# Performance work log

Measured on AMD Instinct MI355X. Metric: run time of the kernel, lower is better.

Reference implementation:

```python
import jax, jax.numpy as jnp
import numpy as np

N = 65536        # collocation points
IN_DIM = 4       # x_dim=3 + is_unsteady=1
DEPTH = 256      # hidden width ('depth' arg)
HID = 5          # width-1 hidden tanh layers
OUT = 3


def setup_inputs() -> dict:
    key = jax.random.key(0)
    ks = jax.random.split(key, 4)
    def init(k, shape, fan_in):
        return jax.random.normal(k, shape, dtype=jnp.float32) / np.sqrt(fan_in).astype(np.float32)
    return {
        "x":  jax.random.normal(ks[0], (N, IN_DIM), dtype=jnp.float32),
        "W0": init(ks[1], (IN_DIM, DEPTH), IN_DIM),
        "b0": jnp.zeros((DEPTH,), jnp.float32),
        "Wh": init(ks[2], (HID, DEPTH, DEPTH), DEPTH),
        "bh": jnp.zeros((HID, DEPTH), jnp.float32),
        "Wl": init(ks[3], (DEPTH, OUT), DEPTH),
        "bl": jnp.zeros((OUT,), jnp.float32),
    }


def _mlp(x, W0, b0, Wh, bh, Wl, bl):
    # Faithful to nn.Sequential: first Linear has NO activation after it,
    # then (width-1) x [Linear, Tanh], then output Linear.
    h = x @ W0 + b0
    for i in range(HID):
        h = jnp.tanh(h @ Wh[i] + bh[i])
    return h @ Wl + bl  # vector potential a: [N, 3]


def reference(x, W0, b0, Wh, bh, Wl, bl):
    # curl(a) via 3 batched reverse-mode pulls (same math as torch autograd.grad
    # with grad_outputs = e_i repeated over the batch).
    a, vjp_fn = jax.vjp(lambda xx: _mlp(xx, W0, b0, Wh, bh, Wl, bl), x)
    e = jnp.eye(OUT, dtype=x.dtype)
    cots = jnp.broadcast_to(e[:, None, :], (OUT, x.shape[0], OUT))  # [3, N, 3]
    J = jax.vmap(lambda c: vjp_fn(c)[0])(cots)                      # [3, N, IN_DIM]
    da0dx, da1dx, da2dx = J[0], J[1], J[2]
    u = jnp.stack([
        da2dx[:, 1] - da1dx[:, 2],
        da0dx[:, 2] - da2dx[:, 0],
        da1dx[:, 0] - da0dx[:, 1],
    ], axis=1)  # [N, 3]
    return u
```

## Files before the change

### kernel.cpp

```cpp
#include <hip/hip_runtime.h>

typedef _Float16 f16;
typedef _Float16 f16x8 __attribute__((ext_vector_type(8)));
typedef float    f32x4 __attribute__((ext_vector_type(4)));

#define OFF_WHP   0u
#define OFF_WLP   655360u
#define OFF_W0P   663552u
#define OFF_B0P   729088u
#define OFF_GP    745472u
#define OFF_BHP   794624u

__device__ __forceinline__ int phi(int kk, int g, int e){
  return (kk*2 + (e>>2))*16 + g*4 + (e&3);
}

__device__ __forceinline__ float tanh_fast(float z){
  float e = __builtin_amdgcn_exp2f(z * 2.885390081777927f);
  return 1.f - 2.f*__builtin_amdgcn_rcpf(e + 1.f);
}

__global__ void prepack(const float* __restrict__ W0, const float* __restrict__ b0,
                        const float* __restrict__ Wh, const float* __restrict__ bh,
                        const float* __restrict__ Wl, unsigned char* __restrict__ ws){
  int tid = blockIdx.x*256 + threadIdx.x;
  f16*   whp = (f16*)(ws + OFF_WHP);
  f16*   wlp = (f16*)(ws + OFF_WLP);
  float* w0p = (float*)(ws + OFF_W0P);
  float* b0p = (float*)(ws + OFF_B0P);
  float* gp  = (float*)(ws + OFF_GP);
  float* bhp = (float*)(ws + OFF_BHP);
  if (tid < 327680){
    int e=tid&7, lane=(tid>>3)&63, kk=(tid>>9)&7, nt=(tid>>12)&15, l=tid>>16;
    int k = phi(kk, lane>>4, e);
    int n = nt*16 + (lane&15);
    whp[tid] = (f16)Wh[(l*256 + k)*256 + n];
  } else if (tid < 331776){
    int t = tid - 327680;
    int e=t&7, lane=(t>>3)&63, kk=t>>9;
    int k = phi(kk, lane>>4, e);
    int n = lane&15;
    wlp[t] = (n<3) ? (f16)Wl[k*3+n] : (f16)0.f;
  } else if (tid < 335872){
    int t = tid - 331776;
    int e=t&7, lane=(t>>3)&63, kk=t>>9;
    int k = phi(kk, lane>>4, e);
    #pragma unroll
    for(int i=0;i<4;i++) w0p[t*4+i] = W0[i*256+k];
    b0p[t] = b0[k];
  } else if (tid < 348160){
    int t = tid - 335872;
    int e=t&7, lane=(t>>3)&63, kk=(t>>9)&7, j=t>>12;
    int k = phi(kk, lane>>4, e);
    float acc = 0.f;
    for(int k0=0;k0<256;k0++) acc = fmaf(W0[j*256+k0], Wh[k0*256+k], acc);
    gp[t] = acc;
  } else if (tid < 368640){
    int t = tid - 348160;
    int r=t&3, lane=(t>>2)&63, nt=(t>>8)&15, l=t>>12;
    bhp[t] = bh[l*256 + nt*16 + (lane>>4)*4 + r];
  }
}

__device__ __forceinline__ int moff(int lane, int kk){
  return lane*128 + ((kk ^ (lane & 7)) << 4);
}

__global__ __launch_bounds__(512, 4) void velcurl(
    const float* __restrict__ x, const unsigned char* __restrict__ ws,
    float* __restrict__ out){
  __shared__ __align__(16) char xbuf[4][8192];
  __shared__ __align__(16) char mbuf[2][8192];
  __shared__ float outt[3][3][16];

  const int lane  = threadIdx.x & 63;
  const int W     = threadIdx.x >> 6;
  const int c     = W & 3;
  const int h     = W >> 2;
  const int s     = lane & 15;
  const int sbase = blockIdx.x << 4;

  const f16x8* __restrict__ whp = (const f16x8*)(ws + OFF_WHP);
  const f16x8* __restrict__ wlp = (const f16x8*)(ws + OFF_WLP);
  const f32x4* __restrict__ w0p = (const f32x4*)(ws + OFF_W0P);
  const float* __restrict__ b0p = (const float*)(ws + OFF_B0P);
  const float* __restrict__ gp  = (const float*)(ws + OFF_GP);
  const f32x4* __restrict__ bhp = (const f32x4*)(ws + OFF_BHP);

  f16x8 st[8];

  if (c==0){
    const f32x4 xv = ((const f32x4*)x)[sbase + s];
    #pragma unroll
    for(int kk=0;kk<8;kk++){
      f16x8 v;
      #pragma unroll
      for(int e=0;e<8;e++){
        f32x4 wv = w0p[(kk*64+lane)*8+e];
        float b  = b0p[(kk*64+lane)*8+e];
        v[e] = (f16)fmaf(xv[3],wv[3], fmaf(xv[2],wv[2], fmaf(xv[1],wv[1], fmaf(xv[0],wv[0], b))));
      }
      st[kk] = v;
    }
    const f32x4* bp = bhp;
    #pragma unroll
    for(int q=0;q<4;q++){
      const int nt0 = 8*h + 2*q;
      f32x4 a0 = {0.f,0.f,0.f,0.f}, a1 = {0.f,0.f,0.f,0.f};
      #pragma unroll
      for(int kk=0;kk<8;kk++){
        f16x8 f0 = whp[((nt0  )*8+kk)*64+lane];
        f16x8 f1 = whp[((nt0+1)*8+kk)*64+lane];
        a0 = __builtin_amdgcn_mfma_f32_16x16x32_f16(f0, st[kk], a0, 0,0,0);
        a1 = __builtin_amdgcn_mfma_f32_16x16x32_f16(f1, st[kk], a1, 0,0,0);
      }
      f32x4 b0v = bp[nt0*64+lane], b1v = bp[(nt0+1)*64+lane];
      f16x8 hv, mv;
      #pragma unroll
      for(int r=0;r<4;r++){
        float h0 = tanh_fast(a0[r]+b0v[r]);
        float h1 = tanh_fast(a1[r]+b1v[r]);
        hv[r] = (f16)h0;  hv[4+r] = (f16)h1;
        mv[r] = (f16)(1.f-h0*h0);  mv[4+r] = (f16)(1.f-h1*h1);
      }
      *(f16x8*)(&xbuf[0][0] + moff(lane, 4*h+q)) = hv;
      *(f16x8*)(&mbuf[0][0] + moff(lane, 4*h+q)) = mv;
    }
  }
  __syncthreads();

  #pragma unroll 1
  for(int p=1;p<5;p++){
    const f16x8* wl = whp + p*8192;
    if (c==0){
      #pragma unroll
      for(int kk=0;kk<8;kk++)
        st[kk] = *(const f16x8*)(&xbuf[0][0] + moff(lane, kk));
    } else if (p==1){
      const int j = c-1;
      const f32x4* gpv = (const f32x4*)gp;
      #pragma unroll
      for(int kk=0;kk<8;kk++){
        f16x8 m8 = *(const f16x8*)(&mbuf[0][0] + moff(lane, kk));
        f32x4 g0 = gpv[((j*8+kk)*64+lane)*2+0];
        f32x4 g1 = gpv[((j*8+kk)*64+lane)*2+1];
        f16x8 v;
        #pragma unroll
        for(int e=0;e<8;e++){
          float gv = (e<4) ? g0[e&3] : g1[e&3];
          v[e] = (f16)((float)m8[e] * gv);
        }
        st[kk] = v;
      }
    } else {
      #pragma unroll
      for(int kk=0;kk<8;kk++){
        f16x8 m8 = *(const f16x8*)(&mbuf[(p-1)&1][0] + moff(lane, kk));
        f16x8 x8 = *(const f16x8*)(&xbuf[c][0] + moff(lane, kk));
        st[kk] = m8 * x8;
      }
    }
    __syncthreads();

    if (c==0){
      const f32x4* bp = bhp + p*1024;
      #pragma unroll
      for(int q=0;q<4;q++){
        const int nt0 = 8*h + 2*q;
        f32x4 a0 = {0.f,0.f,0.f,0.f}, a1 = {0.f,0.f,0.f,0.f};
        #pragma unroll
        for(int kk=0;kk<8;kk++){
          f16x8 f0 = wl[((nt0  )*8+kk)*64+lane];
          f16x8 f1 = wl[((nt0+1)*8+kk)*64+lane];
          a0 = __builtin_amdgcn_mfma_f32_16x16x32_f16(f0, st[kk], a0, 0,0,0);
          a1 = __builtin_amdgcn_mfma_f32_16x16x32_f16(f1, st[kk], a1, 0,0,0);
        }
        f32x4 b0v = bp[nt0*64+lane], b1v = bp[(nt0+1)*64+lane];
        f16x8 hv, mv;
        #pragma unroll
        for(int r=0;r<4;r++){
          float h0 = tanh_fast(a0[r]+b0v[r]);
          float h1 = tanh_fast(a1[r]+b1v[r]);
          hv[r] = (f16)h0;  hv[4+r] = (f16)h1;
          mv[r] = (f16)(1.f-h0*h0);  mv[4+r] = (f16)(1.f-h1*h1);
        }
        *(f16x8*)(&xbuf[0][0] + moff(lane, 4*h+q)) = hv;
        *(f16x8*)(&mbuf[p&1][0] + moff(lane, 4*h+q)) = mv;
      }
    } else {
      #pragma unroll
      for(int q=0;q<4;q++){
        const int nt0 = 8*h + 2*q;
        f32x4 a0 = {0.f,0.f,0.f,0.f}, a1 = {0.f,0.f,0.f,0.f};
        #pragma unroll
        for(int kk=0;kk<8;kk++){
          f16x8 f0 = wl[((nt0  )*8+kk)*64+lane];
          f16x8 f1 = wl[((nt0+1)*8+kk)*64+lane];
          a0 = __builtin_amdgcn_mfma_f32_16x16x32_f16(f0, st[kk], a0, 0,0,0);
          a1 = __builtin_amdgcn_mfma_f32_16x16x32_f16(f1, st[kk], a1, 0,0,0);
        }
        f16x8 v;
        #pragma unroll
        for(int r=0;r<4;r++){ v[r] = (f16)a0[r]; v[4+r] = (f16)a1[r]; }
        *(f16x8*)(&xbuf[c][0] + moff(lane, 4*h+q)) = v;
      }
    }
    __syncthreads();
  }

  if (c>0 && h==0){
    f32x4 acc = {0.f,0.f,0.f,0.f};
    #pragma unroll
    for(int kk=0;kk<8;kk++){
      f16x8 m8 = *(const f16x8*)(&mbuf[0][0] + moff(lane, kk));
      f16x8 x8 = *(const f16x8*)(&xbuf[c][0] + moff(lane, kk));
      acc = __builtin_amdgcn_mfma_f32_16x16x32_f16(wlp[kk*64+lane], m8*x8, acc, 0,0,0);
    }
    if (lane<16){
      outt[c-1][0][lane] = acc[0];
      outt[c-1][1][lane] = acc[1];
      outt[c-1][2][lane] = acc[2];
    }
  }
  __syncthreads();

  if (W==0 && lane<16){
    const int so = (sbase + lane)*3;
    out[so+0] = outt[1][2][lane] - outt[2][1][lane];
    out[so+1] = outt[2][0][lane] - outt[0][2][lane];
    out[so+2] = outt[0][1][lane] - outt[1][0][lane];
  }
}

extern "C" void kernel_launch(void* const* d_in, const int* in_sizes, int n_in,
                              void* d_out, int out_size, void* d_ws, size_t ws_size,
                              hipStream_t stream){
  const float* x  = (const float*)d_in[0];
  const float* W0 = (const float*)d_in[1];
  const float* b0 = (const float*)d_in[2];
  const float* Wh = (const float*)d_in[3];
  const float* bh = (const float*)d_in[4];
  const float* Wl = (const float*)d_in[5];
  prepack<<<1440, 256, 0, stream>>>(W0, b0, Wh, bh, Wl, (unsigned char*)d_ws);
  velcurl<<<4096, 512, 0, stream>>>(x, (const unsigned char*)d_ws, (float*)d_out);
}
```

Before: 451.5 us.

## Use one wave per chain with 256-thread blocks and merge layer-0 into loop

Halves the block to four waves, so each wave computes all 16 output tiles of its chain instead of splitting them between two waves. The first layer is folded into the main loop, removing one barrier, and the q loop is no longer unrolled to reduce register pressure. The aim is less per-block synchronisation and shared-memory traffic. The cost is fewer resident waves per CU, since LDS use per block is unchanged and the launch bound drops to three blocks, so latency hiding may suffer.

After: 624.3 us. 1.38x slower.

```diff
diff --git a/kernel.cpp b/kernel.cpp
--- a/kernel.cpp
+++ b/kernel.cpp
@@ -66,7 +66,7 @@
   return lane*128 + ((kk ^ (lane & 7)) << 4);
 }
 
-__global__ __launch_bounds__(512, 4) void velcurl(
+__global__ __launch_bounds__(256, 3) void velcurl(
     const float* __restrict__ x, const unsigned char* __restrict__ ws,
     float* __restrict__ out){
   __shared__ __align__(16) char xbuf[4][8192];
@@ -74,9 +74,7 @@
   __shared__ float outt[3][3][16];
 
   const int lane  = threadIdx.x & 63;
-  const int W     = threadIdx.x >> 6;
-  const int c     = W & 3;
-  const int h     = W >> 2;
+  const int c     = threadIdx.x >> 6;
   const int s     = lane & 15;
   const int sbase = blockIdx.x << 4;
 
@@ -87,95 +85,72 @@
   const float* __restrict__ gp  = (const float*)(ws + OFF_GP);
   const f32x4* __restrict__ bhp = (const f32x4*)(ws + OFF_BHP);
 
+  char* const xbc = &xbuf[c][0];
   f16x8 st[8];
 
-  if (c==0){
-    const f32x4 xv = ((const f32x4*)x)[sbase + s];
-    #pragma unroll
-    for(int kk=0;kk<8;kk++){
-      f16x8 v;
-      #pragma unroll
-      for(int e=0;e<8;e++){
-        f32x4 wv = w0p[(kk*64+lane)*8+e];
-        float b  = b0p[(kk*64+lane)*8+e];
-        v[e] = (f16)fmaf(xv[3],wv[3], fmaf(xv[2],wv[2], fmaf(xv[1],wv[1], fmaf(xv[0],wv[0], b))));
-      }
-      st[kk] = v;
-    }
-    const f32x4* bp = bhp;
-    #pragma unroll
-    for(int q=0;q<4;q++){
-      const int nt0 = 8*h + 2*q;
-      f32x4 a0 = {0.f,0.f,0.f,0.f}, a1 = {0.f,0.f,0.f,0.f};
-      #pragma unroll
-      for(int kk=0;kk<8;kk++){
-        f16x8 f0 = whp[((nt0  )*8+kk)*64+lane];
-        f16x8 f1 = whp[((nt0+1)*8+kk)*64+lane];
-        a0 = __builtin_amdgcn_mfma_f32_16x16x32_f16(f0, st[kk], a0, 0,0,0);
-        a1 = __builtin_amdgcn_mfma_f32_16x16x32_f16(f1, st[kk], a1, 0,0,0);
-      }
-      f32x4 b0v = bp[nt0*64+lane], b1v = bp[(nt0+1)*64+lane];
-      f16x8 hv, mv;
-      #pragma unroll
-      for(int r=0;r<4;r++){
-        float h0 = tanh_fast(a0[r]+b0v[r]);
-        float h1 = tanh_fast(a1[r]+b1v[r]);
-        hv[r] = (f16)h0;  hv[4+r] = (f16)h1;
-        mv[r] = (f16)(1.f-h0*h0);  mv[4+r] = (f16)(1.f-h1*h1);
-      }
-      *(f16x8*)(&xbuf[0][0] + moff(lane, 4*h+q)) = hv;
-      *(f16x8*)(&mbuf[0][0] + moff(lane, 4*h+q)) = mv;
-    }
-  }
-  __syncthreads();
-
   #pragma unroll 1
-  for(int p=1;p<5;p++){
+  for(int p=0;p<5;p++){
     const f16x8* wl = whp + p*8192;
-    if (c==0){
-      #pragma unroll
-      for(int kk=0;kk<8;kk++)
-        st[kk] = *(const f16x8*)(&xbuf[0][0] + moff(lane, kk));
-    } else if (p==1){
-      const int j = c-1;
-      const f32x4* gpv = (const f32x4*)gp;
-      #pragma unroll
-      for(int kk=0;kk<8;kk++){
-        f16x8 m8 = *(const f16x8*)(&mbuf[0][0] + moff(lane, kk));
-        f32x4 g0 = gpv[((j*8+kk)*64+lane)*2+0];
-        f32x4 g1 = gpv[((j*8+kk)*64+lane)*2+1];
-        f16x8 v;
-        #pragma unroll
-        for(int e=0;e<8;e++){
-          float gv = (e<4) ? g0[e&3] : g1[e&3];
-          v[e] = (f16)((float)m8[e] * gv);
-        }
-        st[kk] = v;
+    if (p==0){
+      if (c==0){
+        const f32x4 xv = ((const f32x4*)x)[sbase + s];
+        #pragma unroll
+        for(int kk=0;kk<8;kk++){
+          f16x8 v;
+          #pragma unroll
+          for(int e=0;e<8;e++){
+            f32x4 wv = w0p[(kk*64+lane)*8+e];
+            float b  = b0p[(kk*64+lane)*8+e];
+            v[e] = (f16)fmaf(xv[3],wv[3], fmaf(xv[2],wv[2], fmaf(xv[1],wv[1], fmaf(xv[0],wv[0], b))));
+          }
+          st[kk] = v;
+        }
       }
     } else {
-      #pragma unroll
-      for(int kk=0;kk<8;kk++){
-        f16x8 m8 = *(const f16x8*)(&mbuf[(p-1)&1][0] + moff(lane, kk));
-        f16x8 x8 = *(const f16x8*)(&xbuf[c][0] + moff(lane, kk));
-        st[kk] = m8 * x8;
-      }
-    }
-    __syncthreads();
+      const char* mb_prev = &mbuf[(p-1)&1][0];
+      if (c==0){
+        #pragma unroll
+        for(int kk=0;kk<8;kk++)
+          st[kk] = *(const f16x8*)(xbc + moff(lane, kk));
+      } else if (p==1){
+        const int j = c-1;
+        const f32x4* gpv = (const f32x4*)gp;
+        #pragma unroll
+        for(int kk=0;kk<8;kk++){
+          f16x8 m8 = *(const f16x8*)(mb_prev + moff(lane, kk));
+          f32x4 g0 = gpv[((j*8+kk)*64+lane)*2+0];
+          f32x4 g1 = gpv[((j*8+kk)*64+lane)*2+1];
+          f16x8 v;
+          #pragma unroll
+          for(int e=0;e<8;e++){
+            float gv = (e<4) ? g0[e&3] : g1[e&3];
+            v[e] = (f16)((float)m8[e] * gv);
+          }
+          st[kk] = v;
+        }
+      } else {
+        #pragma unroll
+        for(int kk=0;kk<8;kk++){
+          f16x8 m8 = *(const f16x8*)(mb_prev + moff(lane, kk));
+          f16x8 x8 = *(const f16x8*)(xbc + moff(lane, kk));
+          st[kk] = m8 * x8;
+        }
+      }
+    }
 
     if (c==0){
       const f32x4* bp = bhp + p*1024;
-      #pragma unroll
-      for(int q=0;q<4;q++){
-        const int nt0 = 8*h + 2*q;
+      char* mb = &mbuf[p&1][0];
+      #pragma unroll 1
+      for(int q=0;q<8;q++){
+        const f16x8* fp = wl + (2*q)*8*64 + lane;
         f32x4 a0 = {0.f,0.f,0.f,0.f}, a1 = {0.f,0.f,0.f,0.f};
         #pragma unroll
         for(int kk=0;kk<8;kk++){
-          f16x8 f0 = wl[((nt0  )*8+kk)*64+lane];
-          f16x8 f1 = wl[((nt0+1)*8+kk)*64+lane];
-          a0 = __builtin_amdgcn_mfma_f32_16x16x32_f16(f0, st[kk], a0, 0,0,0);
-          a1 = __builtin_amdgcn_mfma_f32_16x16x32_f16(f1, st[kk], a1, 0,0,0);
-        }
-        f32x4 b0v = bp[nt0*64+lane], b1v = bp[(nt0+1)*64+lane];
+          a0 = __builtin_amdgcn_mfma_f32_16x16x32_f16(fp[kk*64],     st[kk], a0, 0,0,0);
+          a1 = __builtin_amdgcn_mfma_f32_16x16x32_f16(fp[(8+kk)*64], st[kk], a1, 0,0,0);
+        }
+        f32x4 b0v = bp[(2*q)*64+lane], b1v = bp[(2*q+1)*64+lane];
         f16x8 hv, mv;
         #pragma unroll
         for(int r=0;r<4;r++){
@@ -184,36 +159,35 @@
           hv[r] = (f16)h0;  hv[4+r] = (f16)h1;
           mv[r] = (f16)(1.f-h0*h0);  mv[4+r] = (f16)(1.f-h1*h1);
         }
-        *(f16x8*)(&xbuf[0][0] + moff(lane, 4*h+q)) = hv;
-        *(f16x8*)(&mbuf[p&1][0] + moff(lane, 4*h+q)) = mv;
-      }
-    } else {
-      #pragma unroll
-      for(int q=0;q<4;q++){
-        const int nt0 = 8*h + 2*q;
+        *(f16x8*)(xbc + moff(lane, q)) = hv;
+        *(f16x8*)(mb  + moff(lane, q)) = mv;
+      }
+    } else if (p>=1){
+      #pragma unroll 1
+      for(int q=0;q<8;q++){
+        const f16x8* fp = wl + (2*q)*8*64 + lane;
         f32x4 a0 = {0.f,0.f,0.f,0.f}, a1 = {0.f,0.f,0.f,0.f};
         #pragma unroll
         for(int kk=0;kk<8;kk++){
-          f16x8 f0 = wl[((nt0  )*8+kk)*64+lane];
-          f16x8 f1 = wl[((nt0+1)*8+kk)*64+lane];
-          a0 = __builtin_amdgcn_mfma_f32_16x16x32_f16(f0, st[kk], a0, 0,0,0);
-          a1 = __builtin_amdgcn_mfma_f32_16x16x32_f16(f1, st[kk], a1, 0,0,0);
+          a0 = __builtin_amdgcn_mfma_f32_16x16x32_f16(fp[kk*64],     st[kk], a0, 0,0,0);
+          a1 = __builtin_amdgcn_mfma_f32_16x16x32_f16(fp[(8+kk)*64], st[kk], a1, 0,0,0);
         }
         f16x8 v;
         #pragma unroll
         for(int r=0;r<4;r++){ v[r] = (f16)a0[r]; v[4+r] = (f16)a1[r]; }
-        *(f16x8*)(&xbuf[c][0] + moff(lane, 4*h+q)) = v;
+        *(f16x8*)(xbc + moff(lane, q)) = v;
       }
     }
     __syncthreads();
   }
 
-  if (c>0 && h==0){
+  if (c>0){
+    const char* mb = &mbuf[0][0];
     f32x4 acc = {0.f,0.f,0.f,0.f};
     #pragma unroll
     for(int kk=0;kk<8;kk++){
-      f16x8 m8 = *(const f16x8*)(&mbuf[0][0] + moff(lane, kk));
-      f16x8 x8 = *(const f16x8*)(&xbuf[c][0] + moff(lane, kk));
+      f16x8 m8 = *(const f16x8*)(mb + moff(lane, kk));
+      f16x8 x8 = *(const f16x8*)(xbc + moff(lane, kk));
       acc = __builtin_amdgcn_mfma_f32_16x16x32_f16(wlp[kk*64+lane], m8*x8, acc, 0,0,0);
     }
     if (lane<16){
@@ -224,7 +198,7 @@
   }
   __syncthreads();
 
-  if (W==0 && lane<16){
+  if (c==0 && lane<16){
     const int so = (sbase + lane)*3;
     out[so+0] = outt[1][2][lane] - outt[2][1][lane];
     out[so+1] = outt[2][0][lane] - outt[0][2][lane];
@@ -242,5 +216,5 @@
   const float* bh = (const float*)d_in[4];
   const float* Wl = (const float*)d_in[5];
   prepack<<<1440, 256, 0, stream>>>(W0, b0, Wh, bh, Wl, (unsigned char*)d_ws);
-  velcurl<<<4096, 512, 0, stream>>>(x, (const unsigned char*)d_ws, (float*)d_out);
-}
+  velcurl<<<4096, 256, 0, stream>>>(x, (const unsigned char*)d_ws, (float*)d_out);
+}
```
